# Performance work log

Measured on AMD Instinct MI355X. Metric: run time of the kernel, lower is better.

The kernel has to match this reference:

```python
import jax, jax.numpy as jnp
from jax import lax
import numpy as np

N_POINTS = 2048
EPS = 1e-5  # BatchNorm eps (torch default)


def farthest_point_sample(xyz, npoint):
    """Standard PointNet++ FPS, deterministic init at index 0. xyz: [B,N,3] -> [B,npoint] int32."""
    B, N, _ = xyz.shape

    def step(carry, _):
        dist, far = carry
        centroid = jnp.take_along_axis(xyz, far[:, None, None], axis=1)  # [B,1,3]
        d = jnp.sum((xyz - centroid) ** 2, axis=-1)                      # [B,N]
        dist = jnp.minimum(dist, d)
        new_far = jnp.argmax(dist, axis=-1).astype(jnp.int32)
        return (dist, new_far), far

    init = (jnp.full((B, N), 1e10, xyz.dtype), jnp.zeros((B,), jnp.int32))
    _, idx = lax.scan(step, init, None, length=npoint)
    return idx.T  # [B, npoint]


def conv_bn_relu(x, w, b, g, beta):
    """Pointwise Conv1d + BatchNorm1d (training-mode batch stats) + ReLU. x: [B,C,S], w: [O,C]."""
    y = jnp.einsum('bcs,oc->bos', x, w) + b[None, :, None]
    mu = y.mean(axis=(0, 2), keepdims=True)
    var = y.var(axis=(0, 2), keepdims=True)  # biased variance, as torch BN forward
    y = (y - mu) * lax.rsqrt(var + EPS) * g[None, :, None] + beta[None, :, None]
    return jax.nn.relu(y)


def setup_inputs() -> dict:
    key = jax.random.key(0)
    ks = jax.random.split(key, 4)
    B, N = 32, 65536
    chans = [3, 64, 128, 256]
    inp = {"xyz": jax.random.normal(ks[0], (B, N, 3), jnp.float32)}
    for i in range(3):
        cin, cout = chans[i], chans[i + 1]
        inp[f"w{i}"] = jax.random.normal(ks[i + 1], (cout, cin), jnp.float32) * (1.0 / np.sqrt(cin))
        inp[f"b{i}"] = jnp.zeros((cout,), jnp.float32)
        inp[f"g{i}"] = jnp.ones((cout,), jnp.float32)
        inp[f"be{i}"] = jnp.zeros((cout,), jnp.float32)
    # match arg-name order be{i} -> rename to match signature
    return {
        "xyz": inp["xyz"],
        "w0": inp["w0"], "b0": inp["b0"], "g0": inp["g0"], "be0": inp["be0"],
        "w1": inp["w1"], "b1": inp["b1"], "g1": inp["g1"], "be1": inp["be1"],
        "w2": inp["w2"], "b2": inp["b2"], "g2": inp["g2"], "be2": inp["be2"],
    }


def reference(xyz, w0, b0, g0, be0, w1, b1, g1, be1, w2, b2, g2, be2):
    idx = farthest_point_sample(xyz, N_POINTS)                    # [B,S]
    new_xyz = jnp.take_along_axis(xyz, idx[..., None], axis=1)    # [B,S,3]
    x = new_xyz.transpose(0, 2, 1)                                # [B,3,S]
    x = conv_bn_relu(x, w0, b0, g0, be0)
    x = conv_bn_relu(x, w1, b1, g1, be1)
    x = conv_bn_relu(x, w2, b2, g2, be2)
    features = jnp.max(x, axis=2)                                 # [B,256]
    return new_xyz, features
```

## Files before the change

kernel.cpp:

```cpp
#include <hip/hip_runtime.h>
#include <climits>

#define NPTS 65536
#define NB 32
#define NS 2048
#define NSAMP (NB * NS)
#define EPSBN 1e-5f
#define C1 64
#define C2 128
#define C3 256

#define SUM0 0
#define SQ0 64
#define SUM1 128
#define SQ1 256
#define SUM2 384
#define SQ2 640
#define A0O 896
#define T0O 960
#define A1O 1024
#define T1O 1152
#define A2O 1280
#define T2O 1536
#define STATS_BYTES 3584

#define FPS_T 1024
#define PPT (NPTS / FPS_T)
#define NWAVE (FPS_T / 64)

__global__ __launch_bounds__(FPS_T, 1) void fps_kernel(
    const float* __restrict__ xyz, float* __restrict__ out_xyz) {
  const int b = blockIdx.x;
  const int tid = threadIdx.x;
  const float* __restrict__ P = xyz + (size_t)b * NPTS * 3;
  __shared__ float cs[3];
  __shared__ float wmax[NWAVE];
  __shared__ int nbest[2];

  float dist[PPT];
#pragma unroll
  for (int i = 0; i < PPT; ++i) dist[i] = 1e10f;

  if (tid == 0) {
    cs[0] = P[0]; cs[1] = P[1]; cs[2] = P[2];
    nbest[0] = INT_MAX; nbest[1] = INT_MAX;
  }
  __syncthreads();

  for (int k = 0; k < NS; ++k) {
    const float cx = cs[0], cy = cs[1], cz = cs[2];
    if (tid == 0) {
      float* o = out_xyz + ((size_t)b * NS + k) * 3;
      o[0] = cx; o[1] = cy; o[2] = cz;
    }
    float lm0 = -1.f, lm1 = -1.f, lm2 = -1.f, lm3 = -1.f;
#pragma unroll
    for (int i = 0; i < PPT; ++i) {
      const float* q = P + (size_t)(i * FPS_T + tid) * 3;
      const float dx = q[0] - cx;
      const float dy = q[1] - cy;
      const float dz = q[2] - cz;
      const float d = __fadd_rn(__fadd_rn(__fmul_rn(dx, dx), __fmul_rn(dy, dy)),
                                __fmul_rn(dz, dz));
      const float nd = fminf(dist[i], d);
      dist[i] = nd;
      if ((i & 3) == 0) lm0 = fmaxf(lm0, nd);
      else if ((i & 3) == 1) lm1 = fmaxf(lm1, nd);
      else if ((i & 3) == 2) lm2 = fmaxf(lm2, nd);
      else lm3 = fmaxf(lm3, nd);
    }
    float wm = fmaxf(fmaxf(lm0, lm1), fmaxf(lm2, lm3));
#pragma unroll
    for (int off = 32; off > 0; off >>= 1) wm = fmaxf(wm, __shfl_xor(wm, off, 64));
    if ((tid & 63) == 0) wmax[tid >> 6] = wm;
    const int p = k & 1;
    __syncthreads();
    float gmax = wmax[0];
#pragma unroll
    for (int w = 1; w < NWAVE; ++w) gmax = fmaxf(gmax, wmax[w]);
    if (tid == 0) nbest[p ^ 1] = INT_MAX;
    if (wm == gmax) {
      int myb = INT_MAX;
#pragma unroll
      for (int i = 0; i < PPT; ++i)
        if (dist[i] == gmax) myb = min(myb, i * FPS_T + tid);
      if (myb != INT_MAX) atomicMin(&nbest[p], myb);
    }
    __syncthreads();
    const int nstar = nbest[p];
    if (tid == (nstar & (FPS_T - 1))) {
      const float* q = P + (size_t)nstar * 3;
      cs[0] = q[0]; cs[1] = q[1]; cs[2] = q[2];
    }
    __syncthreads();
  }
}

__device__ __forceinline__ float wredsum(float v) {
#pragma unroll
  for (int off = 32; off > 0; off >>= 1) v += __shfl_xor(v, off, 64);
  return v;
}
__device__ __forceinline__ float wredmax(float v) {
#pragma unroll
  for (int off = 32; off > 0; off >>= 1) v = fmaxf(v, __shfl_xor(v, off, 64));
  return v;
}

__global__ __launch_bounds__(256) void pass1_kernel(const float* __restrict__ sx,
                                                    const float* __restrict__ w0,
                                                    const float* __restrict__ b0,
                                                    float* __restrict__ acc) {
  const int sg = blockIdx.x * 256 + threadIdx.x;
  const int lane = threadIdx.x & 63;
  const float x0 = sx[(size_t)sg * 3 + 0];
  const float x1 = sx[(size_t)sg * 3 + 1];
  const float x2 = sx[(size_t)sg * 3 + 2];
  float aS = 0.f, aQ = 0.f;
#pragma unroll
  for (int o = 0; o < C1; ++o) {
    const float v = b0[o] + w0[o * 3 + 0] * x0 + w0[o * 3 + 1] * x1 + w0[o * 3 + 2] * x2;
    const float s = wredsum(v);
    const float q = wredsum(v * v);
    if (lane == o) { aS = s; aQ = q; }
  }
  atomicAdd(&acc[SUM0 + lane], aS);
  atomicAdd(&acc[SQ0 + lane], aQ);
}

__global__ void fin_kernel(const float* __restrict__ s, const float* __restrict__ q,
                           const float* __restrict__ g, const float* __restrict__ be,
                           float* __restrict__ a, float* __restrict__ t, int C) {
  const int c = threadIdx.x;
  if (c < C) {
    const float mean = s[c] * (1.0f / NSAMP);
    const float var = q[c] * (1.0f / NSAMP) - mean * mean;
    const float ai = g[c] / sqrtf(var + EPSBN);
    a[c] = ai;
    t[c] = be[c] - mean * ai;
  }
}

__global__ __launch_bounds__(256) void pass2_kernel(const float* __restrict__ sx,
    const float* __restrict__ w0, const float* __restrict__ b0,
    const float* __restrict__ a0, const float* __restrict__ t0,
    const float* __restrict__ w1, const float* __restrict__ b1,
    float* __restrict__ acc) {
  const int sg = blockIdx.x * 256 + threadIdx.x;
  const int lane = threadIdx.x & 63;
  const float x0 = sx[(size_t)sg * 3 + 0];
  const float x1 = sx[(size_t)sg * 3 + 1];
  const float x2 = sx[(size_t)sg * 3 + 2];
  float h[C1];
#pragma unroll
  for (int o = 0; o < C1; ++o) {
    const float v = b0[o] + w0[o * 3 + 0] * x0 + w0[o * 3 + 1] * x1 + w0[o * 3 + 2] * x2;
    h[o] = fmaxf(a0[o] * v + t0[o], 0.f);
  }
  float aS[2] = {0.f, 0.f}, aQ[2] = {0.f, 0.f};
#pragma unroll
  for (int j = 0; j < 2; ++j) {
    for (int oo = 0; oo < 64; ++oo) {
      const int o = j * 64 + oo;
      float v0 = b1[o], v1 = 0.f, v2 = 0.f, v3 = 0.f;
#pragma unroll
      for (int c = 0; c < C1; c += 4) {
        v0 += w1[o * C1 + c + 0] * h[c + 0];
        v1 += w1[o * C1 + c + 1] * h[c + 1];
        v2 += w1[o * C1 + c + 2] * h[c + 2];
        v3 += w1[o * C1 + c + 3] * h[c + 3];
      }
      const float v = (v0 + v1) + (v2 + v3);
      const float sS = wredsum(v);
      const float sQ = wredsum(v * v);
      if (lane == oo) { aS[j] = sS; aQ[j] = sQ; }
    }
  }
#pragma unroll
  for (int j = 0; j < 2; ++j) {
    atomicAdd(&acc[SUM1 + j * 64 + lane], aS[j]);
    atomicAdd(&acc[SQ1 + j * 64 + lane], aQ[j]);
  }
}

__global__ __launch_bounds__(256, 1) void pass3_kernel(const float* __restrict__ sx,
    const float* __restrict__ w0, const float* __restrict__ b0,
    const float* __restrict__ a0, const float* __restrict__ t0,
    const float* __restrict__ w1, const float* __restrict__ b1,
    const float* __restrict__ a1, const float* __restrict__ t1,
    const float* __restrict__ w2, const float* __restrict__ b2,
    float* __restrict__ acc) {
  const int sg = blockIdx.x * 256 + threadIdx.x;
  const int lane = threadIdx.x & 63;
  const float x0 = sx[(size_t)sg * 3 + 0];
  const float x1 = sx[(size_t)sg * 3 + 1];
  const float x2 = sx[(size_t)sg * 3 + 2];
  float h[C1];
#pragma unroll
  for (int o = 0; o < C1; ++o) {
    const float v = b0[o] + w0[o * 3 + 0] * x0 + w0[o * 3 + 1] * x1 + w0[o * 3 + 2] * x2;
    h[o] = fmaxf(a0[o] * v + t0[o], 0.f);
  }
  float f[C2];
#pragma unroll
  for (int o = 0; o < C2; ++o) {
    float v0 = b1[o], v1 = 0.f, v2 = 0.f, v3 = 0.f;
#pragma unroll
    for (int c = 0; c < C1; c += 4) {
      v0 += w1[o * C1 + c + 0] * h[c + 0];
      v1 += w1[o * C1 + c + 1] * h[c + 1];
      v2 += w1[o * C1 + c + 2] * h[c + 2];
      v3 += w1[o * C1 + c + 3] * h[c + 3];
    }
    const float v = (v0 + v1) + (v2 + v3);
    f[o] = fmaxf(a1[o] * v + t1[o], 0.f);
  }
  float aS[4] = {0, 0, 0, 0}, aQ[4] = {0, 0, 0, 0};
#pragma unroll
  for (int j = 0; j < 4; ++j) {
    for (int oo = 0; oo < 64; ++oo) {
      const int o = j * 64 + oo;
      float v0 = b2[o], v1 = 0.f, v2 = 0.f, v3 = 0.f;
#pragma unroll
      for (int c = 0; c < C2; c += 4) {
        v0 += w2[o * C2 + c + 0] * f[c + 0];
        v1 += w2[o * C2 + c + 1] * f[c + 1];
        v2 += w2[o * C2 + c + 2] * f[c + 2];
        v3 += w2[o * C2 + c + 3] * f[c + 3];
      }
      const float v = (v0 + v1) + (v2 + v3);
      const float sS = wredsum(v);
      const float sQ = wredsum(v * v);
      if (lane == oo) { aS[j] = sS; aQ[j] = sQ; }
    }
  }
#pragma unroll
  for (int j = 0; j < 4; ++j) {
    atomicAdd(&acc[SUM2 + j * 64 + lane], aS[j]);
    atomicAdd(&acc[SQ2 + j * 64 + lane], aQ[j]);
  }
}

__global__ __launch_bounds__(256, 1) void pass4_kernel(const float* __restrict__ sx,
    const float* __restrict__ w0, const float* __restrict__ b0,
    const float* __restrict__ a0, const float* __restrict__ t0,
    const float* __restrict__ w1, const float* __restrict__ b1,
    const float* __restrict__ a1, const float* __restrict__ t1,
    const float* __restrict__ w2, const float* __restrict__ b2,
    const float* __restrict__ a2, const float* __restrict__ t2,
    float* __restrict__ feat) {
  const int sg = blockIdx.x * 256 + threadIdx.x;
  const int lane = threadIdx.x & 63;
  const float x0 = sx[(size_t)sg * 3 + 0];
  const float x1 = sx[(size_t)sg * 3 + 1];
  const float x2 = sx[(size_t)sg * 3 + 2];
  float h[C1];
#pragma unroll
  for (int o = 0; o < C1; ++o) {
    const float v = b0[o] + w0[o * 3 + 0] * x0 + w0[o * 3 + 1] * x1 + w0[o * 3 + 2] * x2;
    h[o] = fmaxf(a0[o] * v + t0[o], 0.f);
  }
  float f[C2];
#pragma unroll
  for (int o = 0; o < C2; ++o) {
    float v0 = b1[o], v1 = 0.f, v2 = 0.f, v3 = 0.f;
#pragma unroll
    for (int c = 0; c < C1; c += 4) {
      v0 += w1[o * C1 + c + 0] * h[c + 0];
      v1 += w1[o * C1 + c + 1] * h[c + 1];
      v2 += w1[o * C1 + c + 2] * h[c + 2];
      v3 += w1[o * C1 + c + 3] * h[c + 3];
    }
    const float v = (v0 + v1) + (v2 + v3);
    f[o] = fmaxf(a1[o] * v + t1[o], 0.f);
  }
  float fm[4] = {0, 0, 0, 0};
#pragma unroll
  for (int j = 0; j < 4; ++j) {
    for (int oo = 0; oo < 64; ++oo) {
      const int o = j * 64 + oo;
      float v0 = b2[o], v1 = 0.f, v2 = 0.f, v3 = 0.f;
#pragma unroll
      for (int c = 0; c < C2; c += 4) {
        v0 += w2[o * C2 + c + 0] * f[c + 0];
        v1 += w2[o * C2 + c + 1] * f[c + 1];
        v2 += w2[o * C2 + c + 2] * f[c + 2];
        v3 += w2[o * C2 + c + 3] * f[c + 3];
      }
      const float v = (v0 + v1) + (v2 + v3);
      const float z = fmaxf(a2[o] * v + t2[o], 0.f);
      const float m = wredmax(z);
      if (lane == oo) fm[j] = m;
    }
  }
  const int b = sg >> 11;
  unsigned* fb = (unsigned*)feat + (size_t)b * C3;
#pragma unroll
  for (int j = 0; j < 4; ++j)
    atomicMax(&fb[j * 64 + lane], __float_as_uint(fm[j]));
}

extern "C" void kernel_launch(void* const* d_in, const int* in_sizes, int n_in,
                              void* d_out, int out_size, void* d_ws, size_t ws_size,
                              hipStream_t stream) {
  const float* xyz = (const float*)d_in[0];
  const float* w0 = (const float*)d_in[1];
  const float* b0 = (const float*)d_in[2];
  const float* g0 = (const float*)d_in[3];
  const float* be0 = (const float*)d_in[4];
  const float* w1 = (const float*)d_in[5];
  const float* b1 = (const float*)d_in[6];
  const float* g1 = (const float*)d_in[7];
  const float* be1 = (const float*)d_in[8];
  const float* w2 = (const float*)d_in[9];
  const float* b2 = (const float*)d_in[10];
  const float* g2 = (const float*)d_in[11];
  const float* be2 = (const float*)d_in[12];

  float* out = (float*)d_out;
  float* nx = out;
  float* feat = out + (size_t)NB * NS * 3;
  float* acc = (float*)d_ws;

  hipMemsetAsync(acc, 0, STATS_BYTES, stream);
  hipMemsetAsync(feat, 0, (size_t)NB * C3 * 4, stream);

  fps_kernel<<<NB, FPS_T, 0, stream>>>(xyz, nx);

  const int nblk = NSAMP / 256;
  pass1_kernel<<<nblk, 256, 0, stream>>>(nx, w0, b0, acc);
  fin_kernel<<<1, C1, 0, stream>>>(acc + SUM0, acc + SQ0, g0, be0, acc + A0O, acc + T0O, C1);
  pass2_kernel<<<nblk, 256, 0, stream>>>(nx, w0, b0, acc + A0O, acc + T0O, w1, b1, acc);
  fin_kernel<<<1, C2, 0, stream>>>(acc + SUM1, acc + SQ1, g1, be1, acc + A1O, acc + T1O, C2);
  pass3_kernel<<<nblk, 256, 0, stream>>>(nx, w0, b0, acc + A0O, acc + T0O, w1, b1,
                                         acc + A1O, acc + T1O, w2, b2, acc);
  fin_kernel<<<1, C3, 0, stream>>>(acc + SUM2, acc + SQ2, g2, be2, acc + A2O, acc + T2O, C3);
  pass4_kernel<<<nblk, 256, 0, stream>>>(nx, w0, b0, acc + A0O, acc + T0O, w1, b1,
                                         acc + A1O, acc + T1O, w2, b2,
                                         acc + A2O, acc + T2O, feat);
}
```

Baseline: 38.84 ms.

## Shrink FPS block to 256 threads and narrow argmax search to matching lanes

Cuts the FPS block from 1024 to 256 threads, so each thread keeps 256 distances in registers and each iteration uses fewer waves and cheaper barriers. The per-thread max is now compared directly instead of the wave max, so only threads that actually hold the global max search for its index. That search is split by the four strided partial maxima and only scans the matching stripes. This risks register spilling with 256 live floats per thread. Some stripe scans are also run twice, which is redundant but harmless for correctness.

```diff
diff --git a/kernel.cpp b/kernel.cpp
--- a/kernel.cpp
+++ b/kernel.cpp
@@ -24,7 +24,7 @@
 #define T2O 1536
 #define STATS_BYTES 3584
 
-#define FPS_T 1024
+#define FPS_T 256
 #define PPT (NPTS / FPS_T)
 #define NWAVE (FPS_T / 64)
 
@@ -69,7 +69,8 @@
       else if ((i & 3) == 2) lm2 = fmaxf(lm2, nd);
       else lm3 = fmaxf(lm3, nd);
     }
-    float wm = fmaxf(fmaxf(lm0, lm1), fmaxf(lm2, lm3));
+    const float wmt = fmaxf(fmaxf(lm0, lm1), fmaxf(lm2, lm3));
+    float wm = wmt;
 #pragma unroll
     for (int off = 32; off > 0; off >>= 1) wm = fmaxf(wm, __shfl_xor(wm, off, 64));
     if ((tid & 63) == 0) wmax[tid >> 6] = wm;
@@ -79,11 +80,43 @@
 #pragma unroll
     for (int w = 1; w < NWAVE; ++w) gmax = fmaxf(gmax, wmax[w]);
     if (tid == 0) nbest[p ^ 1] = INT_MAX;
-    if (wm == gmax) {
+    if (wmt == gmax) {
       int myb = INT_MAX;
-#pragma unroll
-      for (int i = 0; i < PPT; ++i)
-        if (dist[i] == gmax) myb = min(myb, i * FPS_T + tid);
+      if (lm0 == gmax) {
+#pragma unroll
+        for (int i = 0; i < PPT; i += 4)
+          if (dist[i] == gmax) myb = min(myb, i * FPS_T + tid);
+      }
+      if (lm1 == gmax && myb == INT_MAX) {
+#pragma unroll
+        for (int i = 1; i < PPT; i += 4)
+          if (dist[i] == gmax) myb = min(myb, i * FPS_T + tid);
+      }
+      if (lm2 == gmax && myb == INT_MAX) {
+#pragma unroll
+        for (int i = 2; i < PPT; i += 4)
+          if (dist[i] == gmax) myb = min(myb, i * FPS_T + tid);
+      }
+      if (lm3 == gmax && myb == INT_MAX) {
+#pragma unroll
+        for (int i = 3; i < PPT; i += 4)
+          if (dist[i] == gmax) myb = min(myb, i * FPS_T + tid);
+      }
+      if (lm1 == gmax) {
+#pragma unroll
+        for (int i = 1; i < PPT; i += 4)
+          if (dist[i] == gmax) myb = min(myb, i * FPS_T + tid);
+      }
+      if (lm2 == gmax) {
+#pragma unroll
+        for (int i = 2; i < PPT; i += 4)
+          if (dist[i] == gmax) myb = min(myb, i * FPS_T + tid);
+      }
+      if (lm3 == gmax) {
+#pragma unroll
+        for (int i = 3; i < PPT; i += 4)
+          if (dist[i] == gmax) myb = min(myb, i * FPS_T + tid);
+      }
       if (myb != INT_MAX) atomicMin(&nbest[p], myb);
     }
     __syncthreads();
```

Measured after the change: 51.75 ms. 33.3% more time.

## Shrink FPS block to 256 threads, split distances between registers and LDS

Applied to the files above, without the earlier changes.

The FPS kernel now runs 256 threads per block instead of 1024, so each thread owns 256 points. It keeps 192 running min-distances in registers and 64 in a shared-memory array. The argmax tie search scans only the partition whose local max matches the global max. The intent is cheaper per-iteration barriers and reductions with fewer waves, at the cost of fewer threads hiding global-load latency, high register pressure and extra LDS traffic.

```diff
diff --git a/kernel.cpp b/kernel.cpp
--- a/kernel.cpp
+++ b/kernel.cpp
@@ -24,8 +24,9 @@
 #define T2O 1536
 #define STATS_BYTES 3584
 
-#define FPS_T 1024
-#define PPT (NPTS / FPS_T)
+#define FPS_T 256
+#define RPTS 192
+#define LPTS 64
 #define NWAVE (FPS_T / 64)
 
 __global__ __launch_bounds__(FPS_T, 1) void fps_kernel(
@@ -36,10 +37,13 @@
   __shared__ float cs[3];
   __shared__ float wmax[NWAVE];
   __shared__ int nbest[2];
-
-  float dist[PPT];
-#pragma unroll
-  for (int i = 0; i < PPT; ++i) dist[i] = 1e10f;
+  __shared__ float dl[LPTS][FPS_T];
+
+  float dr[RPTS];
+#pragma unroll
+  for (int i = 0; i < RPTS; ++i) dr[i] = 1e10f;
+#pragma unroll
+  for (int j = 0; j < LPTS; ++j) dl[j][tid] = 1e10f;
 
   if (tid == 0) {
     cs[0] = P[0]; cs[1] = P[1]; cs[2] = P[2];
@@ -53,23 +57,36 @@
       float* o = out_xyz + ((size_t)b * NS + k) * 3;
       o[0] = cx; o[1] = cy; o[2] = cz;
     }
-    float lm0 = -1.f, lm1 = -1.f, lm2 = -1.f, lm3 = -1.f;
-#pragma unroll
-    for (int i = 0; i < PPT; ++i) {
+    float lm0 = -1.f, lm1 = -1.f;
+#pragma unroll
+    for (int i = 0; i < RPTS; ++i) {
       const float* q = P + (size_t)(i * FPS_T + tid) * 3;
       const float dx = q[0] - cx;
       const float dy = q[1] - cy;
       const float dz = q[2] - cz;
       const float d = __fadd_rn(__fadd_rn(__fmul_rn(dx, dx), __fmul_rn(dy, dy)),
                                 __fmul_rn(dz, dz));
-      const float nd = fminf(dist[i], d);
-      dist[i] = nd;
-      if ((i & 3) == 0) lm0 = fmaxf(lm0, nd);
-      else if ((i & 3) == 1) lm1 = fmaxf(lm1, nd);
-      else if ((i & 3) == 2) lm2 = fmaxf(lm2, nd);
-      else lm3 = fmaxf(lm3, nd);
-    }
-    float wm = fmaxf(fmaxf(lm0, lm1), fmaxf(lm2, lm3));
+      const float nd = fminf(dr[i], d);
+      dr[i] = nd;
+      if (i & 1) lm1 = fmaxf(lm1, nd); else lm0 = fmaxf(lm0, nd);
+    }
+    float lm2 = -1.f, lm3 = -1.f;
+#pragma unroll
+    for (int j = 0; j < LPTS; ++j) {
+      const float* q = P + (size_t)((RPTS + j) * FPS_T + tid) * 3;
+      const float dx = q[0] - cx;
+      const float dy = q[1] - cy;
+      const float dz = q[2] - cz;
+      const float d = __fadd_rn(__fadd_rn(__fmul_rn(dx, dx), __fmul_rn(dy, dy)),
+                                __fmul_rn(dz, dz));
+      const float nd = fminf(dl[j][tid], d);
+      dl[j][tid] = nd;
+      if (j & 1) lm3 = fmaxf(lm3, nd); else lm2 = fmaxf(lm2, nd);
+    }
+    const float lmr = fmaxf(lm0, lm1);
+    const float lml = fmaxf(lm2, lm3);
+    const float wmt = fmaxf(lmr, lml);
+    float wm = wmt;
 #pragma unroll
     for (int off = 32; off > 0; off >>= 1) wm = fmaxf(wm, __shfl_xor(wm, off, 64));
     if ((tid & 63) == 0) wmax[tid >> 6] = wm;
@@ -79,11 +96,18 @@
 #pragma unroll
     for (int w = 1; w < NWAVE; ++w) gmax = fmaxf(gmax, wmax[w]);
     if (tid == 0) nbest[p ^ 1] = INT_MAX;
-    if (wm == gmax) {
+    if (wmt == gmax) {
       int myb = INT_MAX;
-#pragma unroll
-      for (int i = 0; i < PPT; ++i)
-        if (dist[i] == gmax) myb = min(myb, i * FPS_T + tid);
+      if (lmr == gmax) {
+#pragma unroll
+        for (int i = 0; i < RPTS; ++i)
+          if (dr[i] == gmax) myb = min(myb, i * FPS_T + tid);
+      }
+      if (lml == gmax) {
+#pragma unroll
+        for (int j = 0; j < LPTS; ++j)
+          if (dl[j][tid] == gmax) myb = min(myb, (RPTS + j) * FPS_T + tid);
+      }
       if (myb != INT_MAX) atomicMin(&nbest[p], myb);
     }
     __syncthreads();
```

Result: slower. 51.33 ms (+32.2%).
